# Kernel optimization log

Measured on AMD Instinct MI355X. Metric: run time of the kernel, lower is better.

The kernel has to match this reference:

```python
import jax, jax.numpy as jnp
import numpy as np
from jax import lax

ALPHA = 0.42
POOL = 7  # avg_pool2d kernel size (count_include_pad=True -> divide by 49 always)

# fixed 3x3 kernels stacked as [out=3, in=1, 3, 3]: sobel_x, sobel_y, laplacian
_SOBEL_X = np.array([[1, 0, -1], [2, 0, -2], [1, 0, -1]], dtype=np.float32)
_SOBEL_Y = np.array([[1, 2, 1], [0, 0, 0], [-1, -2, -1]], dtype=np.float32)
_LAP = np.array([[0, 1, 0], [1, -4, 1], [0, 1, 0]], dtype=np.float32)
_KERNELS = jnp.asarray(np.stack([_SOBEL_X, _SOBEL_Y, _LAP])[:, None])  # [3,1,3,3]


def setup_inputs() -> dict:
    key = jax.random.key(0)
    k1, k2 = jax.random.split(key)
    logits = jax.random.normal(k1, (16, 3, 1024, 1024), dtype=jnp.float32)
    learnable_weights = jax.random.uniform(k2, (3,), dtype=jnp.float32) * 0.1
    return {"logits": logits, "learnable_weights": learnable_weights}


def _avg_pool_same(x):
    # x: [N, H, W]; torch avg_pool2d(kernel=7, stride=1, padding=3, count_include_pad=True)
    s = lax.reduce_window(x, 0.0, lax.add, (1, POOL, POOL), (1, 1, 1), "SAME")
    return s / (POOL * POOL)


def reference(logits, learnable_weights):
    B, S, H, W = logits.shape
    probs = jax.nn.sigmoid(logits)
    m = probs.reshape(B * S, 1, H, W)  # fold slices into batch -> one grouped conv
    # single conv producing gx, gy, laplacian channels
    conv = lax.conv_general_dilated(
        m, _KERNELS, window_strides=(1, 1), padding="SAME",
        dimension_numbers=("NCHW", "OIHW", "NCHW"))  # [B*S, 3, H, W]
    gx, gy, lp = conv[:, 0], conv[:, 1], conv[:, 2]
    edge = jnp.sqrt(gx * gx + gy * gy) + 0.5 * jnp.abs(lp)  # [B*S, H, W]
    m0 = m[:, 0]
    local_mean = _avg_pool_same(m0)
    local_var = _avg_pool_same((m0 - local_mean) ** 2)
    score = ALPHA * edge.sum((1, 2)) + (1.0 - ALPHA) * local_var.sum((1, 2))
    edge_scores = score.reshape(B, S)
    w_edge = edge_scores / (edge_scores.sum(1, keepdims=True) + 1e-6)
    w_learn = jax.nn.softmax(learnable_weights)  # [S]
    weights = (w_edge + w_learn[None, :]) * 0.5  # [B, S]
    fused = jnp.einsum("bshw,bs->bhw", logits, weights)
    return fused
```

## Files before the change

kernel.cpp:

```cpp
#include <hip/hip_runtime.h>
#include <math.h>

#define ALPHA 0.42f
#define H 1024
#define W 1024
#define NB 16
#define NCH 48
#define BH 32

typedef float nfloat4 __attribute__((ext_vector_type(4)));

__device__ __forceinline__ float sigf(float x) {
    return 1.0f / (1.0f + __expf(-x));
}

__global__ __launch_bounds__(256, 2)
void score_kernel(const float* __restrict__ logits, float* __restrict__ scores) {
    __shared__ float red[4];
    const int tid  = threadIdx.x;
    const int lane = tid & 63;
    const int wvi  = tid >> 6;
    const int ch   = blockIdx.y;
    const int band = blockIdx.x * BH;
    const int gx0  = wvi * 256 + lane * 4;
    const float* img = logits + (size_t)ch * (H * W);

    const bool isL = (lane == 0);
    const bool isR = (lane == 63);
    const bool haloActive = isL || isR;
    const int  hx_raw = isL ? (gx0 - 4) : (gx0 + 4);
    const bool hValid = (hx_raw >= 0) && (hx_raw <= W - 4);
    const int  hx = min(max(hx_raw, 0), W - 4);

    const float fxf0 = (float)(7 - max(0, 3 - (gx0 + 0)) - max(0, (gx0 + 0) - (W - 4)));
    const float fxf1 = (float)(7 - max(0, 3 - (gx0 + 1)) - max(0, (gx0 + 1) - (W - 4)));
    const float fxf2 = (float)(7 - max(0, 3 - (gx0 + 2)) - max(0, (gx0 + 2) - (W - 4)));
    const float fxf3 = (float)(7 - max(0, 3 - (gx0 + 3)) - max(0, (gx0 + 3) - (W - 4)));

    float4 vb[4];
    float4 hb[4];
    float srm[8], sr0[8], sr1[8], sr2[8], sr3[8], srp[8];
    float rsA[8], rsB[8], rsC[8], rsD[8];
    float vs0 = 0.f, vs1 = 0.f, vs2 = 0.f, vs3 = 0.f;
    float acc = 0.f;
    #pragma unroll
    for (int k = 0; k < 8; ++k) { rsA[k] = rsB[k] = rsC[k] = rsD[k] = 0.f; }

    auto LOAD = [&](int g, int slot4) {
        int gc = min(max(g, 0), H - 1);
        const float* p = img + (size_t)gc * W;
        vb[slot4] = *(const float4*)(p + gx0);
        if (haloActive) hb[slot4] = *(const float4*)(p + hx);
    };

    auto INGEST = [&](int g, int slot4, int slot8) {
        float4 raw = vb[slot4];
        bool rowv = (g >= 0) && (g < H);
        float s0v = 0.f, s1v = 0.f, s2v = 0.f, s3v = 0.f;
        if (rowv) { s0v = sigf(raw.x); s1v = sigf(raw.y); s2v = sigf(raw.z); s3v = sigf(raw.w); }
        float l1 = __shfl_up(s1v, 1), l2 = __shfl_up(s2v, 1), l3 = __shfl_up(s3v, 1);
        float r0 = __shfl_down(s0v, 1), r1 = __shfl_down(s1v, 1), r2 = __shfl_down(s2v, 1);
        if (haloActive) {
            float4 h = hb[slot4];
            bool hv = hValid && rowv;
            float h0 = hv ? sigf(h.x) : 0.f;
            float h1 = hv ? sigf(h.y) : 0.f;
            float h2 = hv ? sigf(h.z) : 0.f;
            float h3 = hv ? sigf(h.w) : 0.f;
            if (isL) { l1 = h1; l2 = h2; l3 = h3; }
            else     { r0 = h0; r1 = h1; r2 = h2; }
        }
        float a = l1 + l2 + l3 + s0v + s1v + s2v + s3v;
        float b = a - l1 + r0;
        float c = b - l2 + r1;
        float d = c - l3 + r2;
        int old = (slot8 + 1) & 7;
        vs0 += a - rsA[old]; vs1 += b - rsB[old];
        vs2 += c - rsC[old]; vs3 += d - rsD[old];
        rsA[slot8] = a; rsB[slot8] = b; rsC[slot8] = c; rsD[slot8] = d;
        srm[slot8] = l3; sr0[slot8] = s0v; sr1[slot8] = s1v;
        sr2[slot8] = s2v; sr3[slot8] = s3v; srp[slot8] = r0;
    };

#define PIX(a00,a01,a02,a10,a11,a12,a20,a21,a22,vsv,fx) do {            \
        float sgx = ((a00) - (a02)) + 2.f * ((a10) - (a12)) + ((a20) - (a22)); \
        float sgy = ((a00) + 2.f * (a01) + (a02)) - ((a20) + 2.f * (a21) + (a22)); \
        float lp  = (a01) + (a10) + (a12) + (a21) - 4.f * (a11);        \
        float edge = sqrtf(sgx * sgx + sgy * sgy) + 0.5f * fabsf(lp);   \
        float mean = (vsv) * (1.f / 49.f);                              \
        float dd = (a11) - mean;                                        \
        acc += ALPHA * edge + wvv * (fx) * (dd * dd);                   \
    } while (0)

    auto EMIT = [&](int y, int sA, int sB, int sC) {
        int Y = band + y;
        float wvv = (1.0f - ALPHA) * (1.0f / 49.0f) *
                    (float)(7 - max(0, 3 - Y) - max(0, Y - (H - 4)));
        float A0 = srm[sA], A1 = sr0[sA], A2 = sr1[sA], A3 = sr2[sA], A4 = sr3[sA], A5 = srp[sA];
        float B0 = srm[sB], B1 = sr0[sB], B2 = sr1[sB], B3 = sr2[sB], B4 = sr3[sB], B5 = srp[sB];
        float C0 = srm[sC], C1 = sr0[sC], C2 = sr1[sC], C3 = sr2[sC], C4 = sr3[sC], C5 = srp[sC];
        PIX(A0, A1, A2, B0, B1, B2, C0, C1, C2, vs0, fxf0);
        PIX(A1, A2, A3, B1, B2, B3, C1, C2, C3, vs1, fxf1);
        PIX(A2, A3, A4, B2, B3, B4, C2, C3, C4, vs2, fxf2);
        PIX(A3, A4, A5, B3, B4, B5, C3, C4, C5, vs3, fxf3);
    };

    LOAD(band - 3, 0);
    LOAD(band - 2, 1);
    LOAD(band - 1, 2); INGEST(band - 3, 0, 0);
    LOAD(band + 0, 3); INGEST(band - 2, 1, 1);
    LOAD(band + 1, 0); INGEST(band - 1, 2, 2);
    LOAD(band + 2, 1); INGEST(band + 0, 3, 3);
    LOAD(band + 3, 2); INGEST(band + 1, 0, 4);
    LOAD(band + 4, 3); INGEST(band + 2, 1, 5);

    for (int nn = 8; nn < 8 + BH; nn += 8) {
        #pragma unroll
        for (int k = 0; k < 8; ++k) {
            int n = nn + k;
            if (n <= BH + 5) LOAD(band - 3 + n, k & 3);
            INGEST(band - 5 + n, (k - 2) & 3, (k - 2) & 7);
            EMIT(n - 8, (k + 2) & 7, (k + 3) & 7, (k + 4) & 7);
        }
    }

    #pragma unroll
    for (int off = 32; off > 0; off >>= 1) acc += __shfl_down(acc, off);
    if (lane == 0) red[wvi] = acc;
    __syncthreads();
    if (tid == 0) atomicAdd(&scores[ch], red[0] + red[1] + red[2] + red[3]);
#undef PIX
}

__global__ __launch_bounds__(256)
void fuse_kernel(const float* __restrict__ logits,
                 const float* __restrict__ scores,
                 const float* __restrict__ lw,
                 float* __restrict__ out) {
    const size_t HW4 = (size_t)(H * W) / 4;

    float l0 = lw[0], l1 = lw[1], l2 = lw[2];
    float mx = fmaxf(l0, fmaxf(l1, l2));
    float e0 = __expf(l0 - mx), e1 = __expf(l1 - mx), e2 = __expf(l2 - mx);
    float inv = 1.f / (e0 + e1 + e2);
    float wl0 = e0 * inv, wl1 = e1 * inv, wl2 = e2 * inv;

    size_t t = (size_t)blockIdx.x * 256 + threadIdx.x;
    #pragma unroll
    for (int it = 0; it < 2; ++it) {
        size_t i = t + ((size_t)it << 21);
        size_t b = i >> 18;
        size_t r = i & (HW4 - 1);
        float s0 = scores[b * 3 + 0], s1 = scores[b * 3 + 1], s2 = scores[b * 3 + 2];
        float itot = 1.f / (s0 + s1 + s2 + 1e-6f);
        float w0 = 0.5f * (s0 * itot + wl0);
        float w1 = 0.5f * (s1 * itot + wl1);
        float w2 = 0.5f * (s2 * itot + wl2);
        const nfloat4* base = (const nfloat4*)logits + b * 3 * HW4 + r;
        nfloat4 x0 = __builtin_nontemporal_load(base);
        nfloat4 x1 = __builtin_nontemporal_load(base + HW4);
        nfloat4 x2 = __builtin_nontemporal_load(base + 2 * HW4);
        nfloat4 o = x0 * w0 + x1 * w1 + x2 * w2;
        __builtin_nontemporal_store(o, (nfloat4*)out + i);
    }
}

extern "C" void kernel_launch(void* const* d_in, const int* in_sizes, int n_in,
                              void* d_out, int out_size, void* d_ws, size_t ws_size,
                              hipStream_t stream) {
    const float* logits = (const float*)d_in[0];
    const float* lw     = (const float*)d_in[1];
    float* out    = (float*)d_out;
    float* scores = (float*)d_ws;

    (void)hipMemsetAsync(d_ws, 0, NCH * sizeof(float), stream);

    dim3 g1(H / BH, NCH);
    score_kernel<<<g1, 256, 0, stream>>>(logits, scores);

    fuse_kernel<<<8192, 256, 0, stream>>>(logits, scores, lw, out);
}
```

Baseline: 408.5 us.

## Share row halos through LDS, double band height, restructure fuse kernel loads

The score kernel now gets column halos by writing each sigmoid row to a shared-memory row buffer and reading neighbours back after a barrier. This replaces the extra halo loads and lane shuffles of the edge lanes. The band height doubles to cut vertical halo re-reads, occupancy hint rises to 3, and sigmoid/sqrt use fast rcp/sqrt intrinsics. The fuse kernel hoists the per-batch weight computation per block, processes 4 vectors per thread with normal (cached) loads, and halves the grid. The trade-off is a block-wide barrier on every row step, which may stall the pipeline.

```diff
diff --git a/kernel.cpp b/kernel.cpp
--- a/kernel.cpp
+++ b/kernel.cpp
@@ -6,130 +6,133 @@
 #define W 1024
 #define NB 16
 #define NCH 48
-#define BH 32
+#define BH 64
 
 typedef float nfloat4 __attribute__((ext_vector_type(4)));
 
 __device__ __forceinline__ float sigf(float x) {
-    return 1.0f / (1.0f + __expf(-x));
+    return __builtin_amdgcn_rcpf(1.0f + __expf(-x));
 }
 
-__global__ __launch_bounds__(256, 2)
+__device__ __forceinline__ void block_sync_lds() {
+    asm volatile("s_waitcnt lgkmcnt(0)" ::: "memory");
+    __builtin_amdgcn_s_barrier();
+    asm volatile("" ::: "memory");
+}
+
+__global__ __launch_bounds__(256, 3)
 void score_kernel(const float* __restrict__ logits, float* __restrict__ scores) {
+    __shared__ __align__(16) float lrow[2][1032];
     __shared__ float red[4];
     const int tid  = threadIdx.x;
     const int lane = tid & 63;
     const int wvi  = tid >> 6;
     const int ch   = blockIdx.y;
     const int band = blockIdx.x * BH;
-    const int gx0  = wvi * 256 + lane * 4;
-    const float* img = logits + (size_t)ch * (H * W);
+    const int c4   = wvi * 256 + lane * 4;
+    const float* img   = logits + (size_t)ch * (H * W);
+    const float* gbase = img + c4;
 
-    const bool isL = (lane == 0);
-    const bool isR = (lane == 63);
-    const bool haloActive = isL || isR;
-    const int  hx_raw = isL ? (gx0 - 4) : (gx0 + 4);
-    const bool hValid = (hx_raw >= 0) && (hx_raw <= W - 4);
-    const int  hx = min(max(hx_raw, 0), W - 4);
+    if (tid < 8) {
+        int idx = (tid & 3) + ((tid & 4) ? 1028 : 0);
+        lrow[0][idx] = 0.f;
+        lrow[1][idx] = 0.f;
+    }
 
-    const float fxf0 = (float)(7 - max(0, 3 - (gx0 + 0)) - max(0, (gx0 + 0) - (W - 4)));
-    const float fxf1 = (float)(7 - max(0, 3 - (gx0 + 1)) - max(0, (gx0 + 1) - (W - 4)));
-    const float fxf2 = (float)(7 - max(0, 3 - (gx0 + 2)) - max(0, (gx0 + 2) - (W - 4)));
-    const float fxf3 = (float)(7 - max(0, 3 - (gx0 + 3)) - max(0, (gx0 + 3) - (W - 4)));
+    const float cvar  = (1.0f - ALPHA) * (1.0f / 49.0f);
+    const float wfxc0 = cvar * (float)(7 - max(0, 3 - (c4 + 0)) - max(0, (c4 + 0) - (W - 4)));
+    const float wfxc1 = cvar * (float)(7 - max(0, 3 - (c4 + 1)) - max(0, (c4 + 1) - (W - 4)));
+    const float wfxc2 = cvar * (float)(7 - max(0, 3 - (c4 + 2)) - max(0, (c4 + 2) - (W - 4)));
+    const float wfxc3 = cvar * (float)(7 - max(0, 3 - (c4 + 3)) - max(0, (c4 + 3) - (W - 4)));
 
-    float4 vb[4];
-    float4 hb[4];
+    float4 vb[2];
     float srm[8], sr0[8], sr1[8], sr2[8], sr3[8], srp[8];
     float rsA[8], rsB[8], rsC[8], rsD[8];
-    float vs0 = 0.f, vs1 = 0.f, vs2 = 0.f, vs3 = 0.f;
-    float acc = 0.f;
+    float vs0 = 0.f, vs1 = 0.f, vs2 = 0.f, vs3 = 0.f, acc = 0.f;
     #pragma unroll
     for (int k = 0; k < 8; ++k) { rsA[k] = rsB[k] = rsC[k] = rsD[k] = 0.f; }
 
-    auto LOAD = [&](int g, int slot4) {
+    auto LOADROW = [&](int g, int slot) {
         int gc = min(max(g, 0), H - 1);
-        const float* p = img + (size_t)gc * W;
-        vb[slot4] = *(const float4*)(p + gx0);
-        if (haloActive) hb[slot4] = *(const float4*)(p + hx);
+        vb[slot] = *(const float4*)(gbase + ((size_t)gc << 10));
     };
 
-    auto INGEST = [&](int g, int slot4, int slot8) {
-        float4 raw = vb[slot4];
-        bool rowv = (g >= 0) && (g < H);
-        float s0v = 0.f, s1v = 0.f, s2v = 0.f, s3v = 0.f;
-        if (rowv) { s0v = sigf(raw.x); s1v = sigf(raw.y); s2v = sigf(raw.z); s3v = sigf(raw.w); }
-        float l1 = __shfl_up(s1v, 1), l2 = __shfl_up(s2v, 1), l3 = __shfl_up(s3v, 1);
-        float r0 = __shfl_down(s0v, 1), r1 = __shfl_down(s1v, 1), r2 = __shfl_down(s2v, 1);
-        if (haloActive) {
-            float4 h = hb[slot4];
-            bool hv = hValid && rowv;
-            float h0 = hv ? sigf(h.x) : 0.f;
-            float h1 = hv ? sigf(h.y) : 0.f;
-            float h2 = hv ? sigf(h.z) : 0.f;
-            float h3 = hv ? sigf(h.w) : 0.f;
-            if (isL) { l1 = h1; l2 = h2; l3 = h3; }
-            else     { r0 = h0; r1 = h1; r2 = h2; }
+    auto STEP = [&](int n, int s8, int s2, bool doLoad, bool doEmit) {
+        const int g = band - 3 + n;
+        float4 raw = vb[s2];
+        float q0 = 0.f, q1 = 0.f, q2 = 0.f, q3 = 0.f;
+        if (g >= 0 && g < H) {
+            q0 = sigf(raw.x); q1 = sigf(raw.y); q2 = sigf(raw.z); q3 = sigf(raw.w);
         }
-        float a = l1 + l2 + l3 + s0v + s1v + s2v + s3v;
+        *(float4*)&lrow[s2][c4 + 4] = make_float4(q0, q1, q2, q3);
+        if (doLoad) LOADROW(g + 2, s2);
+        block_sync_lds();
+        float4 hl = *(const float4*)&lrow[s2][c4];
+        float4 hr = *(const float4*)&lrow[s2][c4 + 8];
+        float l1 = hl.y, l2 = hl.z, l3 = hl.w;
+        float r0 = hr.x, r1 = hr.y, r2 = hr.z;
+        float a = ((l1 + l2) + (l3 + q0)) + ((q1 + q2) + q3);
         float b = a - l1 + r0;
         float c = b - l2 + r1;
         float d = c - l3 + r2;
-        int old = (slot8 + 1) & 7;
-        vs0 += a - rsA[old]; vs1 += b - rsB[old];
-        vs2 += c - rsC[old]; vs3 += d - rsD[old];
-        rsA[slot8] = a; rsB[slot8] = b; rsC[slot8] = c; rsD[slot8] = d;
-        srm[slot8] = l3; sr0[slot8] = s0v; sr1[slot8] = s1v;
-        sr2[slot8] = s2v; sr3[slot8] = s3v; srp[slot8] = r0;
+        const int old = (s8 + 1) & 7;
+        vs0 += a - rsA[old]; vs1 += b - rsB[old]; vs2 += c - rsC[old]; vs3 += d - rsD[old];
+        rsA[s8] = a; rsB[s8] = b; rsC[s8] = c; rsD[s8] = d;
+        srm[s8] = l3; sr0[s8] = q0; sr1[s8] = q1; sr2[s8] = q2; sr3[s8] = q3; srp[s8] = r0;
+        if (doEmit) {
+            const int Y = g - 3;
+            float fy = (float)(7 - max(0, 3 - Y) - max(0, Y - (H - 4)));
+            float wf0 = fy * wfxc0, wf1 = fy * wfxc1, wf2 = fy * wfxc2, wf3 = fy * wfxc3;
+            const int sA = (s8 + 4) & 7, sB = (s8 + 5) & 7, sC = (s8 + 6) & 7;
+            float A0 = srm[sA], A1 = sr0[sA], A2 = sr1[sA], A3 = sr2[sA], A4 = sr3[sA], A5 = srp[sA];
+            float B0 = srm[sB], B1 = sr0[sB], B2 = sr1[sB], B3 = sr2[sB], B4 = sr3[sB], B5 = srp[sB];
+            float C0 = srm[sC], C1 = sr0[sC], C2 = sr1[sC], C3 = sr2[sC], C4 = sr3[sC], C5 = srp[sC];
+            float t0 = A0 + C0, t1 = A1 + C1, t2 = A2 + C2, t3 = A3 + C3, t4 = A4 + C4, t5 = A5 + C5;
+            float u0 = A0 - C0, u1 = A1 - C1, u2 = A2 - C2, u3 = A3 - C3, u4 = A4 - C4, u5 = A5 - C5;
+            auto PIXF = [&](float tp, float tp1, float tp2, float Bp, float Bp1, float Bp2,
+                            float up, float up1, float up2, float vsv, float wf) {
+                float sgx = (tp - tp2) + 2.f * (Bp - Bp2);
+                float sgy = (up + up2) + 2.f * up1;
+                float lp  = (Bp + Bp2) + tp1 - 4.f * Bp1;
+                float edge = __builtin_amdgcn_sqrtf(sgx * sgx + sgy * sgy) + 0.5f * fabsf(lp);
+                float dd = Bp1 - vsv * (1.f / 49.f);
+                acc += ALPHA * edge + wf * (dd * dd);
+            };
+            PIXF(t0, t1, t2, B0, B1, B2, u0, u1, u2, vs0, wf0);
+            PIXF(t1, t2, t3, B1, B2, B3, u1, u2, u3, vs1, wf1);
+            PIXF(t2, t3, t4, B2, B3, B4, u2, u3, u4, vs2, wf2);
+            PIXF(t3, t4, t5, B3, B4, B5, u3, u4, u5, vs3, wf3);
+        }
     };
 
-#define PIX(a00,a01,a02,a10,a11,a12,a20,a21,a22,vsv,fx) do {            \
-        float sgx = ((a00) - (a02)) + 2.f * ((a10) - (a12)) + ((a20) - (a22)); \
-        float sgy = ((a00) + 2.f * (a01) + (a02)) - ((a20) + 2.f * (a21) + (a22)); \
-        float lp  = (a01) + (a10) + (a12) + (a21) - 4.f * (a11);        \
-        float edge = sqrtf(sgx * sgx + sgy * sgy) + 0.5f * fabsf(lp);   \
-        float mean = (vsv) * (1.f / 49.f);                              \
-        float dd = (a11) - mean;                                        \
-        acc += ALPHA * edge + wvv * (fx) * (dd * dd);                   \
-    } while (0)
-
-    auto EMIT = [&](int y, int sA, int sB, int sC) {
-        int Y = band + y;
-        float wvv = (1.0f - ALPHA) * (1.0f / 49.0f) *
-                    (float)(7 - max(0, 3 - Y) - max(0, Y - (H - 4)));
-        float A0 = srm[sA], A1 = sr0[sA], A2 = sr1[sA], A3 = sr2[sA], A4 = sr3[sA], A5 = srp[sA];
-        float B0 = srm[sB], B1 = sr0[sB], B2 = sr1[sB], B3 = sr2[sB], B4 = sr3[sB], B5 = srp[sB];
-        float C0 = srm[sC], C1 = sr0[sC], C2 = sr1[sC], C3 = sr2[sC], C4 = sr3[sC], C5 = srp[sC];
-        PIX(A0, A1, A2, B0, B1, B2, C0, C1, C2, vs0, fxf0);
-        PIX(A1, A2, A3, B1, B2, B3, C1, C2, C3, vs1, fxf1);
-        PIX(A2, A3, A4, B2, B3, B4, C2, C3, C4, vs2, fxf2);
-        PIX(A3, A4, A5, B3, B4, B5, C3, C4, C5, vs3, fxf3);
-    };
-
-    LOAD(band - 3, 0);
-    LOAD(band - 2, 1);
-    LOAD(band - 1, 2); INGEST(band - 3, 0, 0);
-    LOAD(band + 0, 3); INGEST(band - 2, 1, 1);
-    LOAD(band + 1, 0); INGEST(band - 1, 2, 2);
-    LOAD(band + 2, 1); INGEST(band + 0, 3, 3);
-    LOAD(band + 3, 2); INGEST(band + 1, 0, 4);
-    LOAD(band + 4, 3); INGEST(band + 2, 1, 5);
-
-    for (int nn = 8; nn < 8 + BH; nn += 8) {
+    LOADROW(band - 3, 0);
+    LOADROW(band - 2, 1);
+    STEP(0, 0, 0, true, false);
+    STEP(1, 1, 1, true, false);
+    STEP(2, 2, 0, true, false);
+    STEP(3, 3, 1, true, false);
+    STEP(4, 4, 0, true, false);
+    STEP(5, 5, 1, true, false);
+    STEP(6, 6, 0, true, true);
+    STEP(7, 7, 1, true, true);
+    #pragma unroll 1
+    for (int nn = 8; nn < BH; nn += 8) {
         #pragma unroll
-        for (int k = 0; k < 8; ++k) {
-            int n = nn + k;
-            if (n <= BH + 5) LOAD(band - 3 + n, k & 3);
-            INGEST(band - 5 + n, (k - 2) & 3, (k - 2) & 7);
-            EMIT(n - 8, (k + 2) & 7, (k + 3) & 7, (k + 4) & 7);
-        }
+        for (int k = 0; k < 8; ++k)
+            STEP(nn + k, k, k & 1, true, true);
     }
+    STEP(BH + 0, 0, 0, true,  true);
+    STEP(BH + 1, 1, 1, true,  true);
+    STEP(BH + 2, 2, 0, true,  true);
+    STEP(BH + 3, 3, 1, true,  true);
+    STEP(BH + 4, 4, 0, false, true);
+    STEP(BH + 5, 5, 1, false, true);
 
     #pragma unroll
     for (int off = 32; off > 0; off >>= 1) acc += __shfl_down(acc, off);
     if (lane == 0) red[wvi] = acc;
     __syncthreads();
     if (tid == 0) atomicAdd(&scores[ch], red[0] + red[1] + red[2] + red[3]);
-#undef PIX
 }
 
 __global__ __launch_bounds__(256)
@@ -142,26 +145,27 @@
     float l0 = lw[0], l1 = lw[1], l2 = lw[2];
     float mx = fmaxf(l0, fmaxf(l1, l2));
     float e0 = __expf(l0 - mx), e1 = __expf(l1 - mx), e2 = __expf(l2 - mx);
-    float inv = 1.f / (e0 + e1 + e2);
+    float inv = __builtin_amdgcn_rcpf(e0 + e1 + e2);
     float wl0 = e0 * inv, wl1 = e1 * inv, wl2 = e2 * inv;
 
-    size_t t = (size_t)blockIdx.x * 256 + threadIdx.x;
+    const int b = blockIdx.x >> 8;
+    float s0 = scores[b * 3 + 0], s1 = scores[b * 3 + 1], s2 = scores[b * 3 + 2];
+    float itot = __builtin_amdgcn_rcpf(s0 + s1 + s2 + 1e-6f);
+    float w0 = 0.5f * (s0 * itot + wl0);
+    float w1 = 0.5f * (s1 * itot + wl1);
+    float w2 = 0.5f * (s2 * itot + wl2);
+
+    size_t i0 = (size_t)blockIdx.x * 1024 + threadIdx.x;
+    size_t r  = i0 & (HW4 - 1);
+    const nfloat4* pb = (const nfloat4*)logits + (size_t)b * 3 * HW4 + r;
+    nfloat4* po = (nfloat4*)out + i0;
     #pragma unroll
-    for (int it = 0; it < 2; ++it) {
-        size_t i = t + ((size_t)it << 21);
-        size_t b = i >> 18;
-        size_t r = i & (HW4 - 1);
-        float s0 = scores[b * 3 + 0], s1 = scores[b * 3 + 1], s2 = scores[b * 3 + 2];
-        float itot = 1.f / (s0 + s1 + s2 + 1e-6f);
-        float w0 = 0.5f * (s0 * itot + wl0);
-        float w1 = 0.5f * (s1 * itot + wl1);
-        float w2 = 0.5f * (s2 * itot + wl2);
-        const nfloat4* base = (const nfloat4*)logits + b * 3 * HW4 + r;
-        nfloat4 x0 = __builtin_nontemporal_load(base);
-        nfloat4 x1 = __builtin_nontemporal_load(base + HW4);
-        nfloat4 x2 = __builtin_nontemporal_load(base + 2 * HW4);
+    for (int k = 0; k < 4; ++k) {
+        nfloat4 x0 = pb[k * 256];
+        nfloat4 x1 = pb[k * 256 + HW4];
+        nfloat4 x2 = pb[k * 256 + 2 * HW4];
         nfloat4 o = x0 * w0 + x1 * w1 + x2 * w2;
-        __builtin_nontemporal_store(o, (nfloat4*)out + i);
+        __builtin_nontemporal_store(o, po + k * 256);
     }
 }
 
@@ -178,5 +182,5 @@
     dim3 g1(H / BH, NCH);
     score_kernel<<<g1, 256, 0, stream>>>(logits, scores);
 
-    fuse_kernel<<<8192, 256, 0, stream>>>(logits, scores, lw, out);
+    fuse_kernel<<<4096, 256, 0, stream>>>(logits, scores, lw, out);
 }
```

Result: faster. 333.9 us (-18.3%).
